# Kernel tuning notes

Measured on AMD Instinct MI355X. Metric: run time of the kernel, lower is better.

The kernel has to match this reference:

```python
import jax, jax.numpy as jnp
import numpy as np


def setup_inputs() -> dict:
    key = jax.random.key(0)
    kq, kk, kv = jax.random.split(key, 3)
    n, d = 8192, 32
    return {
        "Q": jax.random.normal(kq, (n, d), dtype=jnp.float32),
        "K": jax.random.normal(kk, (n, d), dtype=jnp.float32),
        "V": jax.random.normal(kv, (n, d), dtype=jnp.float32),
    }


def reference(Q, K, V):
    # FlashAttention-2 tiling with online softmax is mathematically equivalent
    # to full (unscaled, unmasked) softmax attention: O = softmax(Q K^T) V.
    # Note: the original module applies NO 1/sqrt(d) scaling.
    S = jnp.einsum("qd,kd->qk", Q, K)           # [n, n]
    P = jax.nn.softmax(S, axis=-1)                # numerically stable softmax
    return jnp.einsum("qk,kd->qd", P, V)         # [n, d]
```

## Files before the change

kernel.cpp:

```cpp
#include <hip/hip_runtime.h>
#include <hip/hip_bf16.h>

typedef __bf16 bf16x8 __attribute__((ext_vector_type(8)));
typedef __bf16 bf16x4 __attribute__((ext_vector_type(4)));
typedef float  f32x4  __attribute__((ext_vector_type(4)));
typedef unsigned short u16;

static constexpr int N = 8192;
static constexpr int D = 32;
static constexpr float L2E = 1.44269504088896340736f;
static constexpr float MSHIFT = 32.0f;

__global__ __launch_bounds__(256) void prep_kernel(
    const float* __restrict__ Q, const float* __restrict__ K,
    const float* __restrict__ V, u16* __restrict__ Qb, u16* __restrict__ Kb,
    u16* __restrict__ Vt) {
  __shared__ float tile[64][33];
  const int b = blockIdx.x;
  auto pack = [](float x, float y) -> unsigned int {
    u16 ux = __builtin_bit_cast(u16, (__bf16)x);
    u16 uy = __builtin_bit_cast(u16, (__bf16)y);
    return (unsigned int)ux | ((unsigned int)uy << 16);
  };
  if (b < 256) {
    const int i = (b * 256 + threadIdx.x) * 4;
    const float4 q = *reinterpret_cast<const float4*>(Q + i);
    const float4 k = *reinterpret_cast<const float4*>(K + i);
    uint2 qo = { pack(q.x * L2E, q.y * L2E), pack(q.z * L2E, q.w * L2E) };
    uint2 ko = { pack(k.x, k.y), pack(k.z, k.w) };
    *reinterpret_cast<uint2*>(Qb + i) = qo;
    *reinterpret_cast<uint2*>(Kb + i) = ko;
  } else {
    const int r0 = (b - 256) * 64;
    const int row = threadIdx.x >> 2;
    const int c0 = (threadIdx.x & 3) * 8;
    const float4 x0 = *reinterpret_cast<const float4*>(V + (size_t)(r0 + row) * D + c0);
    const float4 x1 = *reinterpret_cast<const float4*>(V + (size_t)(r0 + row) * D + c0 + 4);
    tile[row][c0 + 0] = x0.x; tile[row][c0 + 1] = x0.y;
    tile[row][c0 + 2] = x0.z; tile[row][c0 + 3] = x0.w;
    tile[row][c0 + 4] = x1.x; tile[row][c0 + 5] = x1.y;
    tile[row][c0 + 6] = x1.z; tile[row][c0 + 7] = x1.w;
    __syncthreads();
    const int d = threadIdx.x >> 3;
    const int kc = (threadIdx.x & 7) * 8;
    uint4 o;
    o.x = pack(tile[kc + 0][d], tile[kc + 1][d]);
    o.y = pack(tile[kc + 2][d], tile[kc + 3][d]);
    o.z = pack(tile[kc + 4][d], tile[kc + 5][d]);
    o.w = pack(tile[kc + 6][d], tile[kc + 7][d]);
    *reinterpret_cast<uint4*>(Vt + (size_t)d * N + r0 + kc) = o;
  }
}

__global__ __launch_bounds__(256, 4) void flash_kernel(
    const u16* __restrict__ Qb, const u16* __restrict__ Kb,
    const u16* __restrict__ Vt, float* __restrict__ lP,
    float* __restrict__ OP, int kpb) {
  __shared__ u16 Ks[2][64 * 32];
  __shared__ u16 Vs[2][32 * 64];

  const int tid = threadIdx.x;
  const int lane = tid & 63;
  const int wave = tid >> 6;
  const int a = lane & 15;
  const int g = lane >> 4;
  const int qg = blockIdx.x & 63;
  const int sp = blockIdx.x >> 6;
  const int qr0 = qg * 128 + wave * 32;
  const int k0 = sp * kpb;
  const int nt = kpb >> 6;

  const bf16x8 qfA = *reinterpret_cast<const bf16x8*>(Qb + (qr0 + a) * D + g * 8);
  const bf16x8 qfB = *reinterpret_cast<const bf16x8*>(Qb + (qr0 + 16 + a) * D + g * 8);

  const int krow = tid >> 2;
  const int kslot = (tid & 3) ^ ((krow >> 1) & 3);
  const u16* __restrict__ ksrc = Kb + krow * D + kslot * 8;
  const int vd = tid >> 3;
  const int v16 = tid & 7;
  const int vblk = v16 ^ ((vd >> 1) & 7);
  const bool vswap = (vd & 1) != 0;
  const u16* __restrict__ vsrc = Vt + (size_t)vd * N + vblk * 8;

  const f32x4 minit = {-MSHIFT, -MSHIFT, -MSHIFT, -MSHIFT};
  const f32x4 zero4 = {0.f, 0.f, 0.f, 0.f};
  f32x4 accA0 = zero4, accA1 = zero4, accB0 = zero4, accB1 = zero4;
  float lA = 0.f, lB = 0.f;

  {
    const uint4 kr = *reinterpret_cast<const uint4*>(ksrc + (size_t)k0 * D);
    const uint4 vr = *reinterpret_cast<const uint4*>(vsrc + k0);
    const uint4 vw = vswap ? uint4{vr.z, vr.w, vr.x, vr.y} : vr;
    *reinterpret_cast<uint4*>(&Ks[0][(size_t)tid * 8]) = kr;
    *reinterpret_cast<uint4*>(&Vs[0][(size_t)tid * 8]) = vw;
  }
  uint4 kreg = {0, 0, 0, 0}, vreg = {0, 0, 0, 0};
  if (nt > 1) {
    kreg = *reinterpret_cast<const uint4*>(ksrc + (size_t)(k0 + 64) * D);
    vreg = *reinterpret_cast<const uint4*>(vsrc + k0 + 64);
  }
  __syncthreads();

  for (int t = 0; t < nt; ++t) {
    const int cur = t & 1;
    const int nxt = cur ^ 1;
    if (t + 1 < nt) {
      const uint4 vw = vswap ? uint4{vreg.z, vreg.w, vreg.x, vreg.y} : vreg;
      *reinterpret_cast<uint4*>(&Ks[nxt][(size_t)tid * 8]) = kreg;
      *reinterpret_cast<uint4*>(&Vs[nxt][(size_t)tid * 8]) = vw;
    }
    __builtin_amdgcn_sched_barrier(0);
    if (t + 2 < nt) {
      kreg = *reinterpret_cast<const uint4*>(ksrc + (size_t)(k0 + (t + 2) * 64) * D);
      vreg = *reinterpret_cast<const uint4*>(vsrc + k0 + (t + 2) * 64);
    }
    __builtin_amdgcn_sched_barrier(0);

    bf16x8 kf[4];
#pragma unroll
    for (int t4 = 0; t4 < 4; ++t4) {
      const int row = 16 * t4 + a;
      kf[t4] = *reinterpret_cast<const bf16x8*>(
          &Ks[cur][row * 32 + ((g ^ ((a >> 1) & 3)) << 3)]);
    }
    bf16x4 v0[4], v1[4];
#pragma unroll
    for (int tt = 0; tt < 4; ++tt) {
      const int slot = ((g + 4 * tt) ^ a) << 2;
      v0[tt] = *reinterpret_cast<const bf16x4*>(&Vs[cur][a * 64 + slot]);
      v1[tt] = *reinterpret_cast<const bf16x4*>(&Vs[cur][(16 + a) * 64 + slot]);
    }

    f32x4 sA[4], sB[4];
#pragma unroll
    for (int t4 = 0; t4 < 4; ++t4) {
      sA[t4] = __builtin_amdgcn_mfma_f32_16x16x32_bf16(kf[t4], qfA, minit, 0, 0, 0);
      sB[t4] = __builtin_amdgcn_mfma_f32_16x16x32_bf16(kf[t4], qfB, minit, 0, 0, 0);
    }

    float pA[4][4], pB[4][4];
#pragma unroll
    for (int t4 = 0; t4 < 4; ++t4) {
#pragma unroll
      for (int r = 0; r < 4; ++r) {
        pA[t4][r] = __builtin_amdgcn_exp2f(sA[t4][r]);
        pB[t4][r] = __builtin_amdgcn_exp2f(sB[t4][r]);
        lA += pA[t4][r];
        lB += pB[t4][r];
      }
    }

    const bf16x8 pfA0 = {(__bf16)pA[0][0], (__bf16)pA[0][1], (__bf16)pA[0][2], (__bf16)pA[0][3],
                         (__bf16)pA[1][0], (__bf16)pA[1][1], (__bf16)pA[1][2], (__bf16)pA[1][3]};
    const bf16x8 pfA1 = {(__bf16)pA[2][0], (__bf16)pA[2][1], (__bf16)pA[2][2], (__bf16)pA[2][3],
                         (__bf16)pA[3][0], (__bf16)pA[3][1], (__bf16)pA[3][2], (__bf16)pA[3][3]};
    const bf16x8 pfB0 = {(__bf16)pB[0][0], (__bf16)pB[0][1], (__bf16)pB[0][2], (__bf16)pB[0][3],
                         (__bf16)pB[1][0], (__bf16)pB[1][1], (__bf16)pB[1][2], (__bf16)pB[1][3]};
    const bf16x8 pfB1 = {(__bf16)pB[2][0], (__bf16)pB[2][1], (__bf16)pB[2][2], (__bf16)pB[2][3],
                         (__bf16)pB[3][0], (__bf16)pB[3][1], (__bf16)pB[3][2], (__bf16)pB[3][3]};

    const bf16x8 va00 = __builtin_shufflevector(v0[0], v0[1], 0, 1, 2, 3, 4, 5, 6, 7);
    const bf16x8 va01 = __builtin_shufflevector(v0[2], v0[3], 0, 1, 2, 3, 4, 5, 6, 7);
    const bf16x8 va10 = __builtin_shufflevector(v1[0], v1[1], 0, 1, 2, 3, 4, 5, 6, 7);
    const bf16x8 va11 = __builtin_shufflevector(v1[2], v1[3], 0, 1, 2, 3, 4, 5, 6, 7);

    accA0 = __builtin_amdgcn_mfma_f32_16x16x32_bf16(va00, pfA0, accA0, 0, 0, 0);
    accA1 = __builtin_amdgcn_mfma_f32_16x16x32_bf16(va10, pfA0, accA1, 0, 0, 0);
    accB0 = __builtin_amdgcn_mfma_f32_16x16x32_bf16(va00, pfB0, accB0, 0, 0, 0);
    accB1 = __builtin_amdgcn_mfma_f32_16x16x32_bf16(va10, pfB0, accB1, 0, 0, 0);
    accA0 = __builtin_amdgcn_mfma_f32_16x16x32_bf16(va01, pfA1, accA0, 0, 0, 0);
    accA1 = __builtin_amdgcn_mfma_f32_16x16x32_bf16(va11, pfA1, accA1, 0, 0, 0);
    accB0 = __builtin_amdgcn_mfma_f32_16x16x32_bf16(va01, pfB1, accB0, 0, 0, 0);
    accB1 = __builtin_amdgcn_mfma_f32_16x16x32_bf16(va11, pfB1, accB1, 0, 0, 0);

    __syncthreads();
  }

  lA += __shfl_xor(lA, 16, 64);
  lA += __shfl_xor(lA, 32, 64);
  lB += __shfl_xor(lB, 16, 64);
  lB += __shfl_xor(lB, 32, 64);

  float* obA = OP + (size_t)(sp * N + qr0 + a) * D;
  float* obB = OP + (size_t)(sp * N + qr0 + 16 + a) * D;
#pragma unroll
  for (int r = 0; r < 4; ++r) {
    obA[4 * g + r] = accA0[r];
    obA[16 + 4 * g + r] = accA1[r];
    obB[4 * g + r] = accB0[r];
    obB[16 + 4 * g + r] = accB1[r];
  }
  if (g == 0) {
    lP[sp * N + qr0 + a] = lA;
    lP[sp * N + qr0 + 16 + a] = lB;
  }
}

template <int NS>
__global__ __launch_bounds__(256) void combine_kernel(
    const float* __restrict__ lP, const float* __restrict__ OP,
    float* __restrict__ out) {
  const int idx = blockIdx.x * 256 + threadIdx.x;
  if (idx >= N * D) return;
  const int q = idx >> 5;
  float L = 0.f, o = 0.f;
#pragma unroll
  for (int s = 0; s < NS; ++s) {
    L += lP[s * N + q];
    o += OP[(size_t)s * N * D + idx];
  }
  out[idx] = o / L;
}

extern "C" void kernel_launch(void* const* d_in, const int* in_sizes, int n_in,
                              void* d_out, int out_size, void* d_ws, size_t ws_size,
                              hipStream_t stream) {
  const float* Q = (const float*)d_in[0];
  const float* K = (const float*)d_in[1];
  const float* V = (const float*)d_in[2];
  float* out = (float*)d_out;

  const size_t base = (size_t)3 * N * D * sizeof(u16);
  const size_t per_split = (size_t)N * sizeof(float) + (size_t)N * D * sizeof(float);
  int ns = 16;
  while (ns > 4 && base + (size_t)ns * per_split > ws_size) ns >>= 1;

  u16* Qb = (u16*)d_ws;
  u16* Kb = Qb + N * D;
  u16* Vt = Kb + N * D;
  float* lP = (float*)(Vt + N * D);
  float* OP = lP + ns * N;

  prep_kernel<<<256 + N / 64, 256, 0, stream>>>(Q, K, V, Qb, Kb, Vt);
  flash_kernel<<<64 * ns, 256, 0, stream>>>(Qb, Kb, Vt, lP, OP, N / ns);
  switch (ns) {
    case 16: combine_kernel<16><<<(N * D) / 256, 256, 0, stream>>>(lP, OP, out); break;
    case 8:  combine_kernel<8><<<(N * D) / 256, 256, 0, stream>>>(lP, OP, out); break;
    default: combine_kernel<4><<<(N * D) / 256, 256, 0, stream>>>(lP, OP, out); break;
  }
}
```

Measured before the change: 35.16 us.

## Load K/V tiles directly into LDS via global_load_lds and template split count

Replaces the register-staged double buffer for K and V tiles with direct global-to-LDS loads (global_load_lds, 16 bytes per lane), changing the V swizzle to match the per-wave contiguous LDS layout. The split count becomes a template parameter so the tile loop has a compile-time trip count and is fully unrolled. The row-sum accumulation is split into partial sums to shorten the dependency chain. This removes VGPR staging and ds_write instructions but depends on the async LDS writes being visible after the barrier, and full unrolling may raise code size and register pressure.

```diff
diff --git a/kernel.cpp b/kernel.cpp
--- a/kernel.cpp
+++ b/kernel.cpp
@@ -10,6 +10,12 @@
 static constexpr int D = 32;
 static constexpr float L2E = 1.44269504088896340736f;
 static constexpr float MSHIFT = 32.0f;
+
+__device__ __forceinline__ void gl_lds16(const u16* g, u16* l) {
+  __builtin_amdgcn_global_load_lds(
+      (const __attribute__((address_space(1))) unsigned int*)g,
+      (__attribute__((address_space(3))) unsigned int*)l, 16, 0, 0);
+}
 
 __global__ __launch_bounds__(256) void prep_kernel(
     const float* __restrict__ Q, const float* __restrict__ K,
@@ -52,12 +58,15 @@
   }
 }
 
+template <int NS>
 __global__ __launch_bounds__(256, 4) void flash_kernel(
     const u16* __restrict__ Qb, const u16* __restrict__ Kb,
     const u16* __restrict__ Vt, float* __restrict__ lP,
-    float* __restrict__ OP, int kpb) {
-  __shared__ u16 Ks[2][64 * 32];
-  __shared__ u16 Vs[2][32 * 64];
+    float* __restrict__ OP) {
+  constexpr int KPB = N / NS;
+  constexpr int NT = KPB / 64;
+  __shared__ u16 Ks[2][2048];
+  __shared__ u16 Vs[2][2048];
 
   const int tid = threadIdx.x;
   const int lane = tid & 63;
@@ -67,8 +76,7 @@
   const int qg = blockIdx.x & 63;
   const int sp = blockIdx.x >> 6;
   const int qr0 = qg * 128 + wave * 32;
-  const int k0 = sp * kpb;
-  const int nt = kpb >> 6;
+  const int k0 = sp * KPB;
 
   const bf16x8 qfA = *reinterpret_cast<const bf16x8*>(Qb + (qr0 + a) * D + g * 8);
   const bf16x8 qfB = *reinterpret_cast<const bf16x8*>(Qb + (qr0 + 16 + a) * D + g * 8);
@@ -77,42 +85,27 @@
   const int kslot = (tid & 3) ^ ((krow >> 1) & 3);
   const u16* __restrict__ ksrc = Kb + krow * D + kslot * 8;
   const int vd = tid >> 3;
-  const int v16 = tid & 7;
-  const int vblk = v16 ^ ((vd >> 1) & 7);
-  const bool vswap = (vd & 1) != 0;
-  const u16* __restrict__ vsrc = Vt + (size_t)vd * N + vblk * 8;
+  const int vlb = (tid & 7) ^ (vd & 7);
+  const u16* __restrict__ vsrc = Vt + (size_t)vd * N + vlb * 8;
+  u16* const kdst = &Ks[0][0] + wave * 512;
+  u16* const vdst = &Vs[0][0] + wave * 512;
 
   const f32x4 minit = {-MSHIFT, -MSHIFT, -MSHIFT, -MSHIFT};
   const f32x4 zero4 = {0.f, 0.f, 0.f, 0.f};
   f32x4 accA0 = zero4, accA1 = zero4, accB0 = zero4, accB1 = zero4;
   float lA = 0.f, lB = 0.f;
 
-  {
-    const uint4 kr = *reinterpret_cast<const uint4*>(ksrc + (size_t)k0 * D);
-    const uint4 vr = *reinterpret_cast<const uint4*>(vsrc + k0);
-    const uint4 vw = vswap ? uint4{vr.z, vr.w, vr.x, vr.y} : vr;
-    *reinterpret_cast<uint4*>(&Ks[0][(size_t)tid * 8]) = kr;
-    *reinterpret_cast<uint4*>(&Vs[0][(size_t)tid * 8]) = vw;
-  }
-  uint4 kreg = {0, 0, 0, 0}, vreg = {0, 0, 0, 0};
-  if (nt > 1) {
-    kreg = *reinterpret_cast<const uint4*>(ksrc + (size_t)(k0 + 64) * D);
-    vreg = *reinterpret_cast<const uint4*>(vsrc + k0 + 64);
-  }
+  gl_lds16(ksrc + (size_t)k0 * D, kdst);
+  gl_lds16(vsrc + k0, vdst);
   __syncthreads();
 
-  for (int t = 0; t < nt; ++t) {
+#pragma unroll
+  for (int t = 0; t < NT; ++t) {
     const int cur = t & 1;
-    const int nxt = cur ^ 1;
-    if (t + 1 < nt) {
-      const uint4 vw = vswap ? uint4{vreg.z, vreg.w, vreg.x, vreg.y} : vreg;
-      *reinterpret_cast<uint4*>(&Ks[nxt][(size_t)tid * 8]) = kreg;
-      *reinterpret_cast<uint4*>(&Vs[nxt][(size_t)tid * 8]) = vw;
-    }
-    __builtin_amdgcn_sched_barrier(0);
-    if (t + 2 < nt) {
-      kreg = *reinterpret_cast<const uint4*>(ksrc + (size_t)(k0 + (t + 2) * 64) * D);
-      vreg = *reinterpret_cast<const uint4*>(vsrc + k0 + (t + 2) * 64);
+    if (t + 1 < NT) {
+      const int kb = k0 + (t + 1) * 64;
+      gl_lds16(ksrc + (size_t)kb * D, kdst + (cur ^ 1) * 2048);
+      gl_lds16(vsrc + kb, vdst + (cur ^ 1) * 2048);
     }
     __builtin_amdgcn_sched_barrier(0);
 
@@ -126,9 +119,10 @@
     bf16x4 v0[4], v1[4];
 #pragma unroll
     for (int tt = 0; tt < 4; ++tt) {
-      const int slot = ((g + 4 * tt) ^ a) << 2;
-      v0[tt] = *reinterpret_cast<const bf16x4*>(&Vs[cur][a * 64 + slot]);
-      v1[tt] = *reinterpret_cast<const bf16x4*>(&Vs[cur][(16 + a) * 64 + slot]);
+      const int pb = ((tt << 1) + (g >> 1)) ^ (a & 7);
+      const int off = pb * 8 + (g & 1) * 4;
+      v0[tt] = *reinterpret_cast<const bf16x4*>(&Vs[cur][a * 64 + off]);
+      v1[tt] = *reinterpret_cast<const bf16x4*>(&Vs[cur][(16 + a) * 64 + off]);
     }
 
     f32x4 sA[4], sB[4];
@@ -139,16 +133,22 @@
     }
 
     float pA[4][4], pB[4][4];
+    float psA = 0.f, psB = 0.f;
 #pragma unroll
     for (int t4 = 0; t4 < 4; ++t4) {
+      float sa = 0.f, sb = 0.f;
 #pragma unroll
       for (int r = 0; r < 4; ++r) {
         pA[t4][r] = __builtin_amdgcn_exp2f(sA[t4][r]);
         pB[t4][r] = __builtin_amdgcn_exp2f(sB[t4][r]);
-        lA += pA[t4][r];
-        lB += pB[t4][r];
+        sa += pA[t4][r];
+        sb += pB[t4][r];
       }
-    }
+      psA += sa;
+      psB += sb;
+    }
+    lA += psA;
+    lB += psB;
 
     const bf16x8 pfA0 = {(__bf16)pA[0][0], (__bf16)pA[0][1], (__bf16)pA[0][2], (__bf16)pA[0][3],
                          (__bf16)pA[1][0], (__bf16)pA[1][1], (__bf16)pA[1][2], (__bf16)pA[1][3]};
@@ -232,10 +232,18 @@
   float* OP = lP + ns * N;
 
   prep_kernel<<<256 + N / 64, 256, 0, stream>>>(Q, K, V, Qb, Kb, Vt);
-  flash_kernel<<<64 * ns, 256, 0, stream>>>(Qb, Kb, Vt, lP, OP, N / ns);
   switch (ns) {
-    case 16: combine_kernel<16><<<(N * D) / 256, 256, 0, stream>>>(lP, OP, out); break;
-    case 8:  combine_kernel<8><<<(N * D) / 256, 256, 0, stream>>>(lP, OP, out); break;
-    default: combine_kernel<4><<<(N * D) / 256, 256, 0, stream>>>(lP, OP, out); break;
-  }
-}
+    case 16:
+      flash_kernel<16><<<64 * 16, 256, 0, stream>>>(Qb, Kb, Vt, lP, OP);
+      combine_kernel<16><<<(N * D) / 256, 256, 0, stream>>>(lP, OP, out);
+      break;
+    case 8:
+      flash_kernel<8><<<64 * 8, 256, 0, stream>>>(Qb, Kb, Vt, lP, OP);
+      combine_kernel<8><<<(N * D) / 256, 256, 0, stream>>>(lP, OP, out);
+      break;
+    default:
+      flash_kernel<4><<<64 * 4, 256, 0, stream>>>(Qb, Kb, Vt, lP, OP);
+      combine_kernel<4><<<(N * D) / 256, 256, 0, stream>>>(lP, OP, out);
+      break;
+  }
+}
```

Result: faster. 33.91 us (-3.6%).
